# Kernel optimization log

Hardware: AMD Instinct MI355X
Metric: run time of the kernel (lower is better)

Reference implementation:

```python
import jax, jax.numpy as jnp
import numpy as np

B, TQ, TK, D, H = 4, 2048, 2048, 512, 8
NEG = -1e9
LN_EPS = 1e-3  # Keras LayerNormalization default


def setup_inputs() -> dict:
    key = jax.random.key(0)
    ks = jax.random.split(key, 5)
    s = 0.02
    return {
        "queries": jax.random.normal(ks[0], (B, TQ, D), jnp.float32),
        "keys_in": jax.random.normal(ks[1], (B, TK, D), jnp.float32),
        "Wq": jax.random.normal(ks[2], (D, D), jnp.float32) * s,
        "bq": jnp.zeros((D,), jnp.float32),
        "Wk": jax.random.normal(ks[3], (D, D), jnp.float32) * s,
        "bk": jnp.zeros((D,), jnp.float32),
        "Wv": jax.random.normal(ks[4], (D, D), jnp.float32) * s,
        "bv": jnp.zeros((D,), jnp.float32),
        "gamma": jnp.ones((D,), jnp.float32),
        "beta": jnp.zeros((D,), jnp.float32),
    }


def reference(queries, keys_in, Wq, bq, Wk, bk, Wv, bv, gamma, beta):
    # Dense projections with relu activation (as in the original layer)
    Q = jax.nn.relu(queries @ Wq + bq)   # [B, Tq, D]
    K = jax.nn.relu(keys_in @ Wk + bk)   # [B, Tk, D]
    V = jax.nn.relu(keys_in @ Wv + bv)   # [B, Tk, D]

    b, tq, d = Q.shape
    tk = K.shape[1]
    dh = d // H
    # split_heads: tf.split(axis=-1)+concat(axis=0) == contiguous feature chunks per head
    Qh = Q.reshape(b, tq, H, dh)
    Kh = K.reshape(b, tk, H, dh)
    Vh = V.reshape(b, tk, H, dh)

    scores = jnp.einsum('bqhd,bkhd->bhqk', Qh, Kh) / jnp.sqrt(jnp.float32(dh))

    # key padding mask derived from per-head K content: sum(|K|) > 0 along dh
    kmask = jnp.sum(jnp.abs(Kh), axis=-1) > 0            # [B, Tk, H]
    kmask = jnp.transpose(kmask, (0, 2, 1))              # [B, H, Tk]
    scores = jnp.where(kmask[:, :, None, :], scores, NEG)

    attn = jax.nn.softmax(scores, axis=-1)               # [B, H, Tq, Tk]

    # query mask: zero out attention rows for all-zero query positions
    qmask = (jnp.sum(jnp.abs(Qh), axis=-1) > 0).astype(attn.dtype)  # [B, Tq, H]
    qmask = jnp.transpose(qmask, (0, 2, 1))              # [B, H, Tq]
    attn = attn * qmask[:, :, :, None]

    out = jnp.einsum('bhqk,bkhd->bqhd', attn, Vh).reshape(b, tq, d)

    # residual + LayerNorm (Keras default: last axis, eps=1e-3)
    res = out + queries
    mu = jnp.mean(res, axis=-1, keepdims=True)
    var = jnp.var(res, axis=-1, keepdims=True)
    return (res - mu) * jax.lax.rsqrt(var + LN_EPS) * gamma + beta
```

## Files before the change

### kernel.cpp

```cpp
#include <hip/hip_runtime.h>
#include <cstdint>

#define BB 4
#define TT 2048
#define DD 512
#define HH 8
#define DH 64
#define NT (TT / 64)
#define LOG2E 1.4426950408889634f

using bf16x8 = __attribute__((ext_vector_type(8))) __bf16;
using f32x4  = __attribute__((ext_vector_type(4))) float;
using f32x16 = __attribute__((ext_vector_type(16))) float;
using us8    = __attribute__((ext_vector_type(8))) unsigned short;
using us4    = __attribute__((ext_vector_type(4))) unsigned short;
using u32x2  = __attribute__((ext_vector_type(2))) unsigned int;

typedef const __attribute__((address_space(1))) unsigned int* as1cp;
typedef __attribute__((address_space(3))) unsigned int* as3p;

__device__ __forceinline__ void gload16(const void* g, void* l) {
  __builtin_amdgcn_global_load_lds((as1cp)(uintptr_t)g,
                                   (as3p)(unsigned int)(uintptr_t)l, 16, 0, 0);
}

__device__ __forceinline__ unsigned short f2bf(float x) {
  unsigned int u = __float_as_uint(x);
  u += 0x7fffu + ((u >> 16) & 1u);
  return (unsigned short)(u >> 16);
}
__device__ __forceinline__ float bf2f(unsigned short u) {
  return __uint_as_float(((unsigned int)u) << 16);
}
__device__ __forceinline__ f32x4 MFMA(bf16x8 a, bf16x8 b, f32x4 c) {
  return __builtin_amdgcn_mfma_f32_16x16x32_bf16(a, b, c, 0, 0, 0);
}
__device__ __forceinline__ f32x16 MFMA32(bf16x8 a, bf16x8 b, f32x16 c) {
  return __builtin_amdgcn_mfma_f32_32x32x16_bf16(a, b, c, 0, 0, 0);
}

#define WAITVM(N) asm volatile("s_waitcnt vmcnt(" #N ")" ::: "memory")
#define RAWBAR() asm volatile("s_barrier" ::: "memory")

__global__ __launch_bounds__(256) void prep_kernel(const float4* __restrict__ q,
                                                   const float4* __restrict__ k,
                                                   us4* __restrict__ qb,
                                                   us4* __restrict__ kb,
                                                   const float* __restrict__ Wq,
                                                   const float* __restrict__ Wk,
                                                   const float* __restrict__ Wv,
                                                   unsigned short* __restrict__ Wt) {
  __shared__ float tile[32][33];
  int id = blockIdx.x;
  if (id < 4096) {
    size_t i = (size_t)id * 256 + threadIdx.x;
    float4 a = q[i];
    us4 o; o[0] = f2bf(a.x); o[1] = f2bf(a.y); o[2] = f2bf(a.z); o[3] = f2bf(a.w);
    qb[i] = o;
    float4 b = k[i];
    us4 p; p[0] = f2bf(b.x); p[1] = f2bf(b.y); p[2] = f2bf(b.z); p[3] = f2bf(b.w);
    kb[i] = p;
  } else {
    int id2 = id - 4096;
    int z = id2 >> 8, rem = id2 & 255;
    const float* W = (z == 0) ? Wq : (z == 1) ? Wk : Wv;
    int k0 = (rem & 15) * 32, n0 = (rem >> 4) * 32;
    int r = threadIdx.x >> 5, c = threadIdx.x & 31;
#pragma unroll
    for (int p = 0; p < 4; ++p)
      tile[r + p * 8][c] = W[(size_t)(k0 + r + p * 8) * DD + n0 + c];
    __syncthreads();
    unsigned short* o = Wt + (size_t)z * DD * DD;
#pragma unroll
    for (int p = 0; p < 4; ++p)
      o[(size_t)(n0 + r + p * 8) * DD + k0 + c] = f2bf(tile[c][r + p * 8]);
  }
}

__global__ __launch_bounds__(256) void gemm_proj(const unsigned short* __restrict__ qb,
                                                 const unsigned short* __restrict__ kb,
                                                 const unsigned short* __restrict__ Wt,
                                                 const float* __restrict__ bq,
                                                 const float* __restrict__ bk,
                                                 const float* __restrict__ bv,
                                                 unsigned short* __restrict__ Qp,
                                                 unsigned short* __restrict__ Kp,
                                                 unsigned short* __restrict__ Vp) {
  int z = blockIdx.z;
  const unsigned short* A  = (z == 0) ? qb : kb;
  const unsigned short* Bt = Wt + (size_t)z * DD * DD;
  const float* bias = (z == 0) ? bq : (z == 1) ? bk : bv;
  unsigned short* out = (z == 0) ? Qp : (z == 1) ? Kp : Vp;
  const float osc = (z == 0) ? 0.125f * LOG2E : 1.0f;

  __shared__ __align__(16) unsigned short As[128 * 32];
  __shared__ __align__(16) unsigned short Bs[128 * 32];

  int mb = blockIdx.x * 128, nb = blockIdx.y * 128;
  int w = threadIdx.x >> 6, lane = threadIdx.x & 63;
  int l15 = lane & 15, lg = lane >> 4;
  int wr = (w >> 1) * 64, wc = (w & 1) * 64;

  f32x4 acc[4][4] = {};

  for (int kt = 0; kt < DD / 32; ++kt) {
    int kk = kt * 32;
    int t = threadIdx.x;
#pragma unroll
    for (int it = 0; it < 2; ++it) {
      int c = t + it * 256;
      gload16(A  + (size_t)(mb + (c >> 2)) * DD + kk + (c & 3) * 8, As + c * 8);
      gload16(Bt + (size_t)(nb + (c >> 2)) * DD + kk + (c & 3) * 8, Bs + c * 8);
    }
    __syncthreads();
    bf16x8 af[4], bf[4];
#pragma unroll
    for (int m = 0; m < 4; ++m)
      af[m] = *(const bf16x8*)&As[(wr + m * 16 + l15) * 32 + lg * 8];
#pragma unroll
    for (int n = 0; n < 4; ++n)
      bf[n] = *(const bf16x8*)&Bs[(wc + n * 16 + l15) * 32 + lg * 8];
#pragma unroll
    for (int m = 0; m < 4; ++m)
#pragma unroll
      for (int n = 0; n < 4; ++n)
        acc[m][n] = MFMA(af[m], bf[n], acc[m][n]);
    __syncthreads();
  }

#pragma unroll
  for (int m = 0; m < 4; ++m)
#pragma unroll
    for (int n = 0; n < 4; ++n)
#pragma unroll
      for (int i = 0; i < 4; ++i) {
        int row = mb + wr + m * 16 + lg * 4 + i;
        int col = nb + wc + n * 16 + l15;
        float v = acc[m][n][i] + bias[col];
        out[(size_t)row * DD + col] = f2bf(fmaxf(v, 0.f) * osc);
      }
}

__global__ __launch_bounds__(256) void post_proj(const unsigned short* __restrict__ Qp,
                                                 const unsigned short* __restrict__ Kp,
                                                 const unsigned short* __restrict__ Vp,
                                                 unsigned short* __restrict__ Vt,
                                                 float* __restrict__ qmask,
                                                 uint2* __restrict__ kbits) {
  __shared__ unsigned short tile[64][72];
  int id = blockIdx.x;
  if (id < 1024) {
    int b = id >> 8, k0 = (id & 31) * 64, d0 = ((id >> 5) & 7) * 64;
    int t = threadIdx.x;
    int r = t >> 3, c8 = (t & 7) * 8;
#pragma unroll
    for (int p = 0; p < 2; ++p) {
      int row = r + p * 32;
      us8 v = *(const us8*)&Vp[(size_t)(b * TT + k0 + row) * DD + d0 + c8];
#pragma unroll
      for (int j = 0; j < 8; ++j) tile[row][c8 + j] = v[j];
    }
    __syncthreads();
#pragma unroll
    for (int p = 0; p < 2; ++p) {
      int dr = r + p * 32;
      us8 o;
#pragma unroll
      for (int j = 0; j < 8; ++j) o[j] = tile[c8 + j][dr];
      *(us8*)&Vt[((size_t)b * DD + d0 + dr) * TT + k0 + c8] = o;
    }
  } else {
    int wid = (id - 1024) * 4 + (threadIdx.x >> 6);
    int lane = threadIdx.x & 63;
    int side = wid >> 10;
    int rem = wid & 1023;
    int bh = rem >> 5, tl = rem & 31;
    int b = bh >> 3, h = bh & 7;
    const unsigned short* src =
        (side ? Kp : Qp) + ((size_t)(b * TT + tl * 64 + lane)) * DD + h * DH;
    float s = 0.f;
#pragma unroll
    for (int j = 0; j < 64; j += 8) {
      us8 v = *(const us8*)(src + j);
#pragma unroll
      for (int e = 0; e < 8; ++e) s += bf2f(v[e]);
    }
    if (side == 0) {
      qmask[(size_t)bh * TT + tl * 64 + lane] = (s > 0.f) ? 1.f : 0.f;
    } else {
      unsigned long long mb = __ballot(s > 0.f);
      if (lane == 0)
        kbits[bh * NT + tl] = make_uint2((unsigned int)mb, (unsigned int)(mb >> 32));
    }
  }
}

#define STAGE(tt, pbuf)                                                      \
  {                                                                          \
    int c0_ = threadIdx.x;                                                   \
    _Pragma("unroll")                                                        \
    for (int it_ = 0; it_ < 2; ++it_) {                                      \
      int c_ = c0_ + it_ * 256;                                              \
      int r_ = c_ >> 3, j_ = c_ & 7;                                         \
      int js_ = j_ ^ (r_ & 7);                                               \
      int kr_ = (r_ & ~12) | ((r_ & 4) << 1) | ((r_ & 8) >> 1);              \
      gload16(kg + (size_t)((tt) * 64 + kr_) * DD + js_ * 8,                 \
              &KsBuf[pbuf][(size_t)c_ * 8]);                                 \
      gload16(vg + (size_t)r_ * TT + (tt) * 64 + js_ * 8,                    \
              &VsBuf[pbuf][(size_t)c_ * 8]);                                 \
    }                                                                        \
  }

__global__ __launch_bounds__(256) void attn_kernel(
    const unsigned short* __restrict__ Qp,
    const unsigned short* __restrict__ Kp,
    const unsigned short* __restrict__ Vt,
    const uint2* __restrict__ kbits,
    unsigned short* __restrict__ Opart,
    float2* __restrict__ ml) {
  __shared__ __align__(16) unsigned short KsBuf[2][64 * 64];
  __shared__ __align__(16) unsigned short VsBuf[2][64 * 64];

  const int w = threadIdx.x >> 6;
  const int lane = threadIdx.x & 63;
  const int l31 = lane & 31, h2 = lane >> 5;

  int flat = blockIdx.x;
  int wg = (flat & 7) * 128 + (flat >> 3);
  int s = wg & 1, qt = (wg >> 1) & 15, bh = wg >> 5;
  int h = bh & 7, b = bh >> 3;
  int q0 = qt * 128 + w * 32;

  const unsigned short* qbase =
      Qp + ((size_t)(b * TT + q0 + l31)) * DD + h * DH + h2 * 8;
  bf16x8 qf[4];
#pragma unroll
  for (int kd = 0; kd < 4; ++kd) qf[kd] = *(const bf16x8*)(qbase + kd * 16);

  const unsigned short* kg = Kp + ((size_t)b * TT) * DD + h * DH;
  const unsigned short* vg = Vt + ((size_t)(b * DD + h * DH)) * TT;
  const uint2* kb_ptr = kbits + (size_t)bh * NT;

  f32x16 oat0 = {}, oat1 = {};
  float m_i = -1e30f, l_i = 0.f;

  const int t0 = s * 16, t1 = t0 + 16;
  STAGE(t0, 0);

  for (int t = t0; t < t1; ++t) {
    int pb = t & 1;
    if (t + 1 < t1) {
      STAGE(t + 1, pb ^ 1);
      WAITVM(4);
    } else {
      WAITVM(0);
    }
    RAWBAR();

    const unsigned short* ksb = &KsBuf[pb][0];
    const unsigned short* vsb = &VsBuf[pb][0];

    bf16x8 kf0[4], kf1[4];
#pragma unroll
    for (int kd = 0; kd < 4; ++kd) {
      int j = kd * 2 + h2;
      int x = (j ^ (l31 & 7)) << 3;
      kf0[kd] = *(const bf16x8*)&ksb[l31 * 64 + x];
      kf1[kd] = *(const bf16x8*)&ksb[(32 + l31) * 64 + x];
    }
    f32x16 s0 = {}, s1 = {};
    __builtin_amdgcn_s_setprio(1);
#pragma unroll
    for (int kd = 0; kd < 4; ++kd) s0 = MFMA32(kf0[kd], qf[kd], s0);
#pragma unroll
    for (int kd = 0; kd < 4; ++kd) s1 = MFMA32(kf1[kd], qf[kd], s1);
    __builtin_amdgcn_s_setprio(0);

    uint2 kw = kb_ptr[t];
    if ((kw.x & kw.y) != 0xffffffffu) {
#pragma unroll
      for (int r = 0; r < 16; ++r) {
        int sh = ((r >> 3) << 4) + (h2 << 3) + (r & 7);
        if (!((kw.x >> sh) & 1)) s0[r] = -1e30f;
        if (!((kw.y >> sh) & 1)) s1[r] = -1e30f;
      }
    }

    float x0 = fmaxf(fmaxf(fmaxf(s0[0], s0[1]), fmaxf(s0[2], s0[3])),
                     fmaxf(fmaxf(s0[4], s0[5]), fmaxf(s0[6], s0[7])));
    float x1 = fmaxf(fmaxf(fmaxf(s0[8], s0[9]), fmaxf(s0[10], s0[11])),
                     fmaxf(fmaxf(s0[12], s0[13]), fmaxf(s0[14], s0[15])));
    float x2 = fmaxf(fmaxf(fmaxf(s1[0], s1[1]), fmaxf(s1[2], s1[3])),
                     fmaxf(fmaxf(s1[4], s1[5]), fmaxf(s1[6], s1[7])));
    float x3 = fmaxf(fmaxf(fmaxf(s1[8], s1[9]), fmaxf(s1[10], s1[11])),
                     fmaxf(fmaxf(s1[12], s1[13]), fmaxf(s1[14], s1[15])));
    float pm = fmaxf(fmaxf(x0, x1), fmaxf(x2, x3));
    u32x2 sw = __builtin_amdgcn_permlane32_swap(__float_as_uint(pm),
                                                __float_as_uint(pm), false, false);
    pm = fmaxf(__uint_as_float(sw[0]), __uint_as_float(sw[1]));

    if (__any(pm > m_i + 12.f)) {
      float mn = fmaxf(m_i, pm);
      float al = exp2f(m_i - mn);
      m_i = mn;
      l_i *= al;
#pragma unroll
      for (int r = 0; r < 16; ++r) { oat0[r] *= al; oat1[r] *= al; }
    }

    float a0 = 0.f, a1 = 0.f, a2 = 0.f, a3 = 0.f;
#pragma unroll
    for (int r = 0; r < 8; ++r)  { float p = exp2f(fminf(s0[r] - m_i, 30.f)); s0[r] = p; a0 += p; }
#pragma unroll
    for (int r = 8; r < 16; ++r) { float p = exp2f(fminf(s0[r] - m_i, 30.f)); s0[r] = p; a1 += p; }
#pragma unroll
    for (int r = 0; r < 8; ++r)  { float p = exp2f(fminf(s1[r] - m_i, 30.f)); s1[r] = p; a2 += p; }
#pragma unroll
    for (int r = 8; r < 16; ++r) { float p = exp2f(fminf(s1[r] - m_i, 30.f)); s1[r] = p; a3 += p; }
    float rs = (a0 + a1) + (a2 + a3);
    u32x2 sr = __builtin_amdgcn_permlane32_swap(__float_as_uint(rs),
                                                __float_as_uint(rs), false, false);
    rs = __uint_as_float(sr[0]) + __uint_as_float(sr[1]);
    l_i += rs;

    bf16x8 vf0[4], vf1[4];
#pragma unroll
    for (int ks = 0; ks < 4; ++ks) {
      int j = ks * 2 + h2;
      int x = (j ^ (l31 & 7)) << 3;
      vf0[ks] = *(const bf16x8*)&vsb[l31 * 64 + x];
      vf1[ks] = *(const bf16x8*)&vsb[(32 + l31) * 64 + x];
    }

    bf16x8 pbf[4];
#pragma unroll
    for (int j = 0; j < 8; ++j) {
      pbf[0][j] = (__bf16)s0[j];
      pbf[1][j] = (__bf16)s0[8 + j];
      pbf[2][j] = (__bf16)s1[j];
      pbf[3][j] = (__bf16)s1[8 + j];
    }

    __builtin_amdgcn_s_setprio(1);
#pragma unroll
    for (int ks = 0; ks < 4; ++ks) {
      oat0 = MFMA32(vf0[ks], pbf[ks], oat0);
      oat1 = MFMA32(vf1[ks], pbf[ks], oat1);
    }
    __builtin_amdgcn_s_setprio(0);

    if (t + 1 < t1) RAWBAR();
  }

  if (h2 == 0)
    ml[((size_t)s * 32 + bh) * TT + q0 + l31] = make_float2(m_i, l_i);
  unsigned short* op = Opart + (size_t)s * (32ull * TT * 64) +
                       ((size_t)bh * TT + q0 + l31) * 64;
#pragma unroll
  for (int e = 0; e < 8; ++e) {
    int r = e * 2;
    int d = (r & 3) + 8 * (r >> 2) + 4 * h2;
    unsigned int w0 = f2bf(oat0[r]) | ((unsigned int)f2bf(oat0[r + 1]) << 16);
    *(unsigned int*)(op + d) = w0;
    unsigned int w1 = f2bf(oat1[r]) | ((unsigned int)f2bf(oat1[r + 1]) << 16);
    *(unsigned int*)(op + 32 + d) = w1;
  }
}

__global__ __launch_bounds__(256) void ln_merge(const unsigned short* __restrict__ Opart,
                                                const float2* __restrict__ ml,
                                                const float* __restrict__ qmask,
                                                const float* __restrict__ qin,
                                                const float* __restrict__ gamma,
                                                const float* __restrict__ beta,
                                                float* __restrict__ out) {
  int row = blockIdx.x * 4 + (threadIdx.x >> 6);
  int j = threadIdx.x & 63;
  int b = row >> 11, q = row & (TT - 1);
  int h = j >> 3, bh = b * 8 + h;
  const size_t SSTR = 32ull * TT * 64;
  size_t pidx = ((size_t)bh * TT + q) * 64 + (size_t)(j & 7) * 8;
  us8 o0 = *(const us8*)(Opart + pidx);
  us8 o1 = *(const us8*)(Opart + SSTR + pidx);
  float2 ma = ml[(size_t)bh * TT + q];
  float2 mb = ml[32ull * TT + (size_t)bh * TT + q];
  float M = fmaxf(ma.x, mb.x);
  float w0 = exp2f(ma.x - M), w1 = exp2f(mb.x - M);
  float l = ma.y * w0 + mb.y * w1;
  float qm = qmask[(size_t)bh * TT + q];
  float sc = qm / fmaxf(l, 1e-30f);

  size_t base = (size_t)row * DD + (size_t)j * 8;
  const float4* q4 = (const float4*)(qin + base);
  float4 c = q4[0], d2 = q4[1];
  float qv[8] = {c.x, c.y, c.z, c.w, d2.x, d2.y, d2.z, d2.w};
  float v[8];
#pragma unroll
  for (int e = 0; e < 8; ++e)
    v[e] = (bf2f(o0[e]) * w0 + bf2f(o1[e]) * w1) * sc + qv[e];

  float s = 0.f, s2 = 0.f;
#pragma unroll
  for (int e = 0; e < 8; ++e) { s += v[e]; s2 += v[e] * v[e]; }
#pragma unroll
  for (int xm = 1; xm < 64; xm <<= 1) {
    s += __shfl_xor(s, xm);
    s2 += __shfl_xor(s2, xm);
  }
  float mu = s * (1.0f / DD);
  float var = s2 * (1.0f / DD) - mu * mu;
  float rsd = rsqrtf(var + 1e-3f);
  const float* g = gamma + j * 8;
  const float* bb = beta + j * 8;
  float* ob = out + base;
#pragma unroll
  for (int e = 0; e < 8; ++e) ob[e] = (v[e] - mu) * rsd * g[e] + bb[e];
}

extern "C" void kernel_launch(void* const* d_in, const int* in_sizes, int n_in,
                              void* d_out, int out_size, void* d_ws, size_t ws_size,
                              hipStream_t stream) {
  (void)in_sizes; (void)n_in; (void)out_size; (void)ws_size;
  const float* queries = (const float*)d_in[0];
  const float* keys_in = (const float*)d_in[1];
  const float* Wq = (const float*)d_in[2];
  const float* bq = (const float*)d_in[3];
  const float* Wk = (const float*)d_in[4];
  const float* bk = (const float*)d_in[5];
  const float* Wv = (const float*)d_in[6];
  const float* bv = (const float*)d_in[7];
  const float* gamma = (const float*)d_in[8];
  const float* beta  = (const float*)d_in[9];
  float* out = (float*)d_out;

  char* ws = (char*)d_ws;
  unsigned short* qb = (unsigned short*)(ws);
  unsigned short* kb = (unsigned short*)(ws + (8ull << 20));
  unsigned short* Opart = (unsigned short*)(ws);
  unsigned short* Qp = (unsigned short*)(ws + (16ull << 20));
  unsigned short* Kp = (unsigned short*)(ws + (24ull << 20));
  unsigned short* Vp = (unsigned short*)(ws + (32ull << 20));
  unsigned short* Vt = (unsigned short*)(ws + (40ull << 20));
  unsigned short* Wt = (unsigned short*)(ws + (48ull << 20));
  float* qmaskp = (float*)(ws + (50ull << 20));
  uint2* kbitsp = (uint2*)(ws + (50ull << 20) + (512ull << 10));
  float2* mlp   = (float2*)(ws + (51ull << 20));

  prep_kernel<<<4864, 256, 0, stream>>>((const float4*)queries, (const float4*)keys_in,
                                        (us4*)qb, (us4*)kb, Wq, Wk, Wv, Wt);
  gemm_proj<<<dim3(64, 4, 3), 256, 0, stream>>>(qb, kb, Wt, bq, bk, bv, Qp, Kp, Vp);
  post_proj<<<1536, 256, 0, stream>>>(Qp, Kp, Vp, Vt, qmaskp, kbitsp);
  attn_kernel<<<1024, 256, 0, stream>>>(Qp, Kp, Vt, kbitsp, Opart, mlp);
  ln_merge<<<2048, 256, 0, stream>>>(Opart, mlp, qmaskp, queries, gamma, beta, out);
}
```

Before: 207.1 us.

## Drop split-K attention, double-buffer projection GEMM, write fp32 normalized output

The attention kernel no longer splits the key range in two. Each block now walks all 32 key tiles, normalizes by l and the query mask itself, and writes fp32 output, so the merge step in the layernorm kernel goes away. The projection GEMM gains double-buffered LDS staging with async global-to-LDS loads to overlap loads with MFMA. V fragment loads are hoisted next to K loads, and the exp clamp is removed. Halving the attention grid to 512 blocks lowers parallelism and lengthens each block's serial loop, and the fp32 intermediate doubles O traffic.

Measured after the change: 203.0 us. 2.0% less time.

```diff
diff --git a/kernel.cpp b/kernel.cpp
--- a/kernel.cpp
+++ b/kernel.cpp
@@ -77,6 +77,19 @@
   }
 }
 
+#define GSTAGE(kt2, pbuf)                                                    \
+  {                                                                          \
+    int t_ = threadIdx.x;                                                    \
+    _Pragma("unroll")                                                        \
+    for (int it_ = 0; it_ < 2; ++it_) {                                      \
+      int c_ = t_ + it_ * 256;                                               \
+      gload16(A  + (size_t)(mb + (c_ >> 2)) * DD + (kt2) * 32 + (c_ & 3) * 8,\
+              &As[pbuf][(size_t)c_ * 8]);                                    \
+      gload16(Bt + (size_t)(nb + (c_ >> 2)) * DD + (kt2) * 32 + (c_ & 3) * 8,\
+              &Bs[pbuf][(size_t)c_ * 8]);                                    \
+    }                                                                        \
+  }
+
 __global__ __launch_bounds__(256) void gemm_proj(const unsigned short* __restrict__ qb,
                                                  const unsigned short* __restrict__ kb,
                                                  const unsigned short* __restrict__ Wt,
@@ -93,8 +106,8 @@
   unsigned short* out = (z == 0) ? Qp : (z == 1) ? Kp : Vp;
   const float osc = (z == 0) ? 0.125f * LOG2E : 1.0f;
 
-  __shared__ __align__(16) unsigned short As[128 * 32];
-  __shared__ __align__(16) unsigned short Bs[128 * 32];
+  __shared__ __align__(16) unsigned short As[2][128 * 32];
+  __shared__ __align__(16) unsigned short Bs[2][128 * 32];
 
   int mb = blockIdx.x * 128, nb = blockIdx.y * 128;
   int w = threadIdx.x >> 6, lane = threadIdx.x & 63;
@@ -103,29 +116,31 @@
 
   f32x4 acc[4][4] = {};
 
+  GSTAGE(0, 0);
   for (int kt = 0; kt < DD / 32; ++kt) {
-    int kk = kt * 32;
-    int t = threadIdx.x;
-#pragma unroll
-    for (int it = 0; it < 2; ++it) {
-      int c = t + it * 256;
-      gload16(A  + (size_t)(mb + (c >> 2)) * DD + kk + (c & 3) * 8, As + c * 8);
-      gload16(Bt + (size_t)(nb + (c >> 2)) * DD + kk + (c & 3) * 8, Bs + c * 8);
-    }
-    __syncthreads();
+    int pb2 = kt & 1;
+    if (kt + 1 < DD / 32) {
+      GSTAGE(kt + 1, pb2 ^ 1);
+      WAITVM(4);
+    } else {
+      WAITVM(0);
+    }
+    RAWBAR();
+
     bf16x8 af[4], bf[4];
 #pragma unroll
     for (int m = 0; m < 4; ++m)
-      af[m] = *(const bf16x8*)&As[(wr + m * 16 + l15) * 32 + lg * 8];
+      af[m] = *(const bf16x8*)&As[pb2][(wr + m * 16 + l15) * 32 + lg * 8];
 #pragma unroll
     for (int n = 0; n < 4; ++n)
-      bf[n] = *(const bf16x8*)&Bs[(wc + n * 16 + l15) * 32 + lg * 8];
+      bf[n] = *(const bf16x8*)&Bs[pb2][(wc + n * 16 + l15) * 32 + lg * 8];
 #pragma unroll
     for (int m = 0; m < 4; ++m)
 #pragma unroll
       for (int n = 0; n < 4; ++n)
         acc[m][n] = MFMA(af[m], bf[n], acc[m][n]);
-    __syncthreads();
+
+    if (kt + 1 < DD / 32) RAWBAR();
   }
 
 #pragma unroll
@@ -216,8 +231,8 @@
     const unsigned short* __restrict__ Kp,
     const unsigned short* __restrict__ Vt,
     const uint2* __restrict__ kbits,
-    unsigned short* __restrict__ Opart,
-    float2* __restrict__ ml) {
+    const float* __restrict__ qmask,
+    float* __restrict__ O) {
   __shared__ __align__(16) unsigned short KsBuf[2][64 * 64];
   __shared__ __align__(16) unsigned short VsBuf[2][64 * 64];
 
@@ -226,8 +241,8 @@
   const int l31 = lane & 31, h2 = lane >> 5;
 
   int flat = blockIdx.x;
-  int wg = (flat & 7) * 128 + (flat >> 3);
-  int s = wg & 1, qt = (wg >> 1) & 15, bh = wg >> 5;
+  int wg = (flat & 7) * 64 + (flat >> 3);
+  int qt = wg & 15, bh = wg >> 4;
   int h = bh & 7, b = bh >> 3;
   int q0 = qt * 128 + w * 32;
 
@@ -244,12 +259,11 @@
   f32x16 oat0 = {}, oat1 = {};
   float m_i = -1e30f, l_i = 0.f;
 
-  const int t0 = s * 16, t1 = t0 + 16;
-  STAGE(t0, 0);
-
-  for (int t = t0; t < t1; ++t) {
+  STAGE(0, 0);
+
+  for (int t = 0; t < NT; ++t) {
     int pb = t & 1;
-    if (t + 1 < t1) {
+    if (t + 1 < NT) {
       STAGE(t + 1, pb ^ 1);
       WAITVM(4);
     } else {
@@ -260,14 +274,16 @@
     const unsigned short* ksb = &KsBuf[pb][0];
     const unsigned short* vsb = &VsBuf[pb][0];
 
-    bf16x8 kf0[4], kf1[4];
+    bf16x8 kf0[4], kf1[4], vf0[4], vf1[4];
 #pragma unroll
     for (int kd = 0; kd < 4; ++kd) {
-      int j = kd * 2 + h2;
-      int x = (j ^ (l31 & 7)) << 3;
+      int x = ((kd * 2 + h2) ^ (l31 & 7)) << 3;
       kf0[kd] = *(const bf16x8*)&ksb[l31 * 64 + x];
       kf1[kd] = *(const bf16x8*)&ksb[(32 + l31) * 64 + x];
-    }
+      vf0[kd] = *(const bf16x8*)&vsb[l31 * 64 + x];
+      vf1[kd] = *(const bf16x8*)&vsb[(32 + l31) * 64 + x];
+    }
+
     f32x16 s0 = {}, s1 = {};
     __builtin_amdgcn_s_setprio(1);
 #pragma unroll
@@ -310,28 +326,19 @@
 
     float a0 = 0.f, a1 = 0.f, a2 = 0.f, a3 = 0.f;
 #pragma unroll
-    for (int r = 0; r < 8; ++r)  { float p = exp2f(fminf(s0[r] - m_i, 30.f)); s0[r] = p; a0 += p; }
-#pragma unroll
-    for (int r = 8; r < 16; ++r) { float p = exp2f(fminf(s0[r] - m_i, 30.f)); s0[r] = p; a1 += p; }
-#pragma unroll
-    for (int r = 0; r < 8; ++r)  { float p = exp2f(fminf(s1[r] - m_i, 30.f)); s1[r] = p; a2 += p; }
-#pragma unroll
-    for (int r = 8; r < 16; ++r) { float p = exp2f(fminf(s1[r] - m_i, 30.f)); s1[r] = p; a3 += p; }
+    for (int r = 0; r < 8; ++r)  { float p = exp2f(s0[r] - m_i); s0[r] = p; a0 += p; }
+#pragma unroll
+    for (int r = 8; r < 16; ++r) { float p = exp2f(s0[r] - m_i); s0[r] = p; a1 += p; }
+#pragma unroll
+    for (int r = 0; r < 8; ++r)  { float p = exp2f(s1[r] - m_i); s1[r] = p; a2 += p; }
+#pragma unroll
+    for (int r = 8; r < 16; ++r) { float p = exp2f(s1[r] - m_i); s1[r] = p; a3 += p; }
     float rs = (a0 + a1) + (a2 + a3);
     u32x2 sr = __builtin_amdgcn_permlane32_swap(__float_as_uint(rs),
                                                 __float_as_uint(rs), false, false);
     rs = __uint_as_float(sr[0]) + __uint_as_float(sr[1]);
     l_i += rs;
 
-    bf16x8 vf0[4], vf1[4];
-#pragma unroll
-    for (int ks = 0; ks < 4; ++ks) {
-      int j = ks * 2 + h2;
-      int x = (j ^ (l31 & 7)) << 3;
-      vf0[ks] = *(const bf16x8*)&vsb[l31 * 64 + x];
-      vf1[ks] = *(const bf16x8*)&vsb[(32 + l31) * 64 + x];
-    }
-
     bf16x8 pbf[4];
 #pragma unroll
     for (int j = 0; j < 8; ++j) {
@@ -349,59 +356,40 @@
     }
     __builtin_amdgcn_s_setprio(0);
 
-    if (t + 1 < t1) RAWBAR();
-  }
-
-  if (h2 == 0)
-    ml[((size_t)s * 32 + bh) * TT + q0 + l31] = make_float2(m_i, l_i);
-  unsigned short* op = Opart + (size_t)s * (32ull * TT * 64) +
-                       ((size_t)bh * TT + q0 + l31) * 64;
-#pragma unroll
-  for (int e = 0; e < 8; ++e) {
-    int r = e * 2;
-    int d = (r & 3) + 8 * (r >> 2) + 4 * h2;
-    unsigned int w0 = f2bf(oat0[r]) | ((unsigned int)f2bf(oat0[r + 1]) << 16);
-    *(unsigned int*)(op + d) = w0;
-    unsigned int w1 = f2bf(oat1[r]) | ((unsigned int)f2bf(oat1[r + 1]) << 16);
-    *(unsigned int*)(op + 32 + d) = w1;
-  }
-}
-
-__global__ __launch_bounds__(256) void ln_merge(const unsigned short* __restrict__ Opart,
-                                                const float2* __restrict__ ml,
-                                                const float* __restrict__ qmask,
-                                                const float* __restrict__ qin,
-                                                const float* __restrict__ gamma,
-                                                const float* __restrict__ beta,
-                                                float* __restrict__ out) {
+    if (t + 1 < NT) RAWBAR();
+  }
+
+  float qm = qmask[(size_t)bh * TT + q0 + l31];
+  float sc = qm / fmaxf(l_i, 1e-30f);
+  float* ob = O + ((size_t)(b * TT + q0 + l31)) * DD + h * DH + h2 * 4;
+#pragma unroll
+  for (int qq = 0; qq < 4; ++qq) {
+    float4 v0 = make_float4(oat0[4 * qq + 0] * sc, oat0[4 * qq + 1] * sc,
+                            oat0[4 * qq + 2] * sc, oat0[4 * qq + 3] * sc);
+    *(float4*)(ob + 8 * qq) = v0;
+    float4 v1 = make_float4(oat1[4 * qq + 0] * sc, oat1[4 * qq + 1] * sc,
+                            oat1[4 * qq + 2] * sc, oat1[4 * qq + 3] * sc);
+    *(float4*)(ob + 32 + 8 * qq) = v1;
+  }
+}
+
+__global__ __launch_bounds__(256) void ln_kernel(const float* __restrict__ O,
+                                                 const float* __restrict__ qin,
+                                                 const float* __restrict__ gamma,
+                                                 const float* __restrict__ beta,
+                                                 float* __restrict__ out) {
   int row = blockIdx.x * 4 + (threadIdx.x >> 6);
-  int j = threadIdx.x & 63;
-  int b = row >> 11, q = row & (TT - 1);
-  int h = j >> 3, bh = b * 8 + h;
-  const size_t SSTR = 32ull * TT * 64;
-  size_t pidx = ((size_t)bh * TT + q) * 64 + (size_t)(j & 7) * 8;
-  us8 o0 = *(const us8*)(Opart + pidx);
-  us8 o1 = *(const us8*)(Opart + SSTR + pidx);
-  float2 ma = ml[(size_t)bh * TT + q];
-  float2 mb = ml[32ull * TT + (size_t)bh * TT + q];
-  float M = fmaxf(ma.x, mb.x);
-  float w0 = exp2f(ma.x - M), w1 = exp2f(mb.x - M);
-  float l = ma.y * w0 + mb.y * w1;
-  float qm = qmask[(size_t)bh * TT + q];
-  float sc = qm / fmaxf(l, 1e-30f);
-
-  size_t base = (size_t)row * DD + (size_t)j * 8;
+  int lane = threadIdx.x & 63;
+  size_t base = (size_t)row * DD + lane * 8;
+  const float4* o4 = (const float4*)(O + base);
   const float4* q4 = (const float4*)(qin + base);
-  float4 c = q4[0], d2 = q4[1];
-  float qv[8] = {c.x, c.y, c.z, c.w, d2.x, d2.y, d2.z, d2.w};
+  float4 a = o4[0], b2 = o4[1], c = q4[0], d2 = q4[1];
   float v[8];
-#pragma unroll
-  for (int e = 0; e < 8; ++e)
-    v[e] = (bf2f(o0[e]) * w0 + bf2f(o1[e]) * w1) * sc + qv[e];
-
+  v[0] = a.x + c.x; v[1] = a.y + c.y; v[2] = a.z + c.z; v[3] = a.w + c.w;
+  v[4] = b2.x + d2.x; v[5] = b2.y + d2.y; v[6] = b2.z + d2.z; v[7] = b2.w + d2.w;
   float s = 0.f, s2 = 0.f;
 #pragma unroll
-  for (int e = 0; e < 8; ++e) { s += v[e]; s2 += v[e] * v[e]; }
+  for (int j = 0; j < 8; ++j) { s += v[j]; s2 += v[j] * v[j]; }
 #pragma unroll
   for (int xm = 1; xm < 64; xm <<= 1) {
     s += __shfl_xor(s, xm);
@@ -409,12 +397,12 @@
   }
   float mu = s * (1.0f / DD);
   float var = s2 * (1.0f / DD) - mu * mu;
-  float rsd = rsqrtf(var + 1e-3f);
-  const float* g = gamma + j * 8;
-  const float* bb = beta + j * 8;
+  float rs = rsqrtf(var + 1e-3f);
+  const float* g = gamma + lane * 8;
+  const float* bb = beta + lane * 8;
   float* ob = out + base;
 #pragma unroll
-  for (int e = 0; e < 8; ++e) ob[e] = (v[e] - mu) * rsd * g[e] + bb[e];
+  for (int j = 0; j < 8; ++j) ob[j] = (v[j] - mu) * rs * g[j] + bb[j];
 }
 
 extern "C" void kernel_launch(void* const* d_in, const int* in_sizes, int n_in,
@@ -436,7 +424,7 @@
   char* ws = (char*)d_ws;
   unsigned short* qb = (unsigned short*)(ws);
   unsigned short* kb = (unsigned short*)(ws + (8ull << 20));
-  unsigned short* Opart = (unsigned short*)(ws);
+  float*          O  = (float*)(ws);
   unsigned short* Qp = (unsigned short*)(ws + (16ull << 20));
   unsigned short* Kp = (unsigned short*)(ws + (24ull << 20));
   unsigned short* Vp = (unsigned short*)(ws + (32ull << 20));
@@ -444,12 +432,11 @@
   unsigned short* Wt = (unsigned short*)(ws + (48ull << 20));
   float* qmaskp = (float*)(ws + (50ull << 20));
   uint2* kbitsp = (uint2*)(ws + (50ull << 20) + (512ull << 10));
-  float2* mlp   = (float2*)(ws + (51ull << 20));
 
   prep_kernel<<<4864, 256, 0, stream>>>((const float4*)queries, (const float4*)keys_in,
                                         (us4*)qb, (us4*)kb, Wq, Wk, Wv, Wt);
   gemm_proj<<<dim3(64, 4, 3), 256, 0, stream>>>(qb, kb, Wt, bq, bk, bv, Qp, Kp, Vp);
   post_proj<<<1536, 256, 0, stream>>>(Qp, Kp, Vp, Vt, qmaskp, kbitsp);
-  attn_kernel<<<1024, 256, 0, stream>>>(Qp, Kp, Vt, kbitsp, Opart, mlp);
-  ln_merge<<<2048, 256, 0, stream>>>(Opart, mlp, qmaskp, queries, gamma, beta, out);
-}
+  attn_kernel<<<512, 256, 0, stream>>>(Qp, Kp, Vt, kbitsp, qmaskp, O);
+  ln_kernel<<<2048, 256, 0, stream>>>(O, queries, gamma, beta, out);
+}
```
